# Kernel tuning notes

Measured on AMD Instinct MI355X. Metric: run time of the kernel, lower is better.

Reference implementation:

```python
import jax, jax.numpy as jnp
import numpy as np

NUM_HEADS = 24
HEAD_DIM = 64
SCALE = HEAD_DIM ** -0.5


def setup_inputs() -> dict:
    key = jax.random.key(0)
    ks = jax.random.split(key, 6)
    b, n_img, n_txt = 2, 4096, 128
    c_in, c_out, c_ctx = 1536, 1536, 4096
    x = jax.random.normal(ks[0], (b, n_img, c_in), dtype=jnp.float32)
    context = jax.random.normal(ks[1], (b, n_txt, c_ctx), dtype=jnp.float32)
    # realistic padding mask: first 96 of 128 tokens valid
    context_mask = jnp.broadcast_to(jnp.arange(n_txt) < 96, (b, n_txt))
    # Linear(in, out, bias=False) stored as [in, out] so y = x @ W
    Wq = jax.random.normal(ks[2], (c_in, c_out), dtype=jnp.float32) * (c_in ** -0.5)
    Wk = jax.random.normal(ks[3], (c_ctx, c_out), dtype=jnp.float32) * (c_ctx ** -0.5)
    Wv = jax.random.normal(ks[4], (c_ctx, c_out), dtype=jnp.float32) * (c_ctx ** -0.5)
    Wo = jax.random.normal(ks[5], (c_out, c_out), dtype=jnp.float32) * (c_out ** -0.5)
    return {"x": x, "context": context, "context_mask": context_mask,
            "Wq": Wq, "Wk": Wk, "Wv": Wv, "Wo": Wo}


def reference(x, context, context_mask, Wq, Wk, Wv, Wo):
    b, n, _ = x.shape
    h, d = NUM_HEADS, HEAD_DIM
    # project and split heads: b n (h d) -> b h n d
    q = (x @ Wq).reshape(b, n, h, d).transpose(0, 2, 1, 3)
    k = (context @ Wk).reshape(b, -1, h, d).transpose(0, 2, 1, 3)
    v = (context @ Wv).reshape(b, -1, h, d).transpose(0, 2, 1, 3)
    scores = jnp.einsum('bhid,bhjd->bhij', q, k) * SCALE
    max_neg = -jnp.finfo(scores.dtype).max
    scores = jnp.where(context_mask[:, None, None, :], scores, max_neg)
    attn = jax.nn.softmax(scores, axis=-1)
    out = jnp.einsum('bhij,bhjd->bhid', attn, v)
    out = out.transpose(0, 2, 1, 3).reshape(b, n, h * d)
    return out @ Wo
```

## Files before the change

kernel.cpp:

```cpp
#include <hip/hip_runtime.h>

typedef __attribute__((ext_vector_type(8))) short s8bf;
typedef __attribute__((ext_vector_type(8))) __bf16 v8bf;
typedef __attribute__((ext_vector_type(4))) float f32x4;

__device__ __forceinline__ short f2bf(float f) {
  union { float f; unsigned u; } v; v.f = f;
  unsigned r = v.u + 0x7FFFu + ((v.u >> 16) & 1u);
  return (short)(r >> 16);
}

__device__ __forceinline__ s8bf pack8(float4 a, float4 b) {
  s8bf o;
  o[0] = f2bf(a.x); o[1] = f2bf(a.y); o[2] = f2bf(a.z); o[3] = f2bf(a.w);
  o[4] = f2bf(b.x); o[5] = f2bf(b.y); o[6] = f2bf(b.z); o[7] = f2bf(b.w);
  return o;
}

__device__ __forceinline__ f32x4 mfma16(s8bf a, s8bf b, f32x4 c) {
  return __builtin_amdgcn_mfma_f32_16x16x32_bf16(
      __builtin_bit_cast(v8bf, a), __builtin_bit_cast(v8bf, b), c, 0, 0, 0);
}

__device__ __forceinline__ void gl_lds16(const void* g, void* l) {
  __builtin_amdgcn_global_load_lds(
      (const __attribute__((address_space(1))) unsigned*)g,
      (__attribute__((address_space(3))) unsigned*)l, 16, 0, 0);
}

__global__ __launch_bounds__(256) void cast_k(
    const float* __restrict__ x, const float* __restrict__ ctx,
    const void* __restrict__ msk,
    short* __restrict__ xbf, short* __restrict__ ctxbf, float* __restrict__ bias)
{
  __shared__ int fmt;
  const int blk = blockIdx.x;
  const int t = threadIdx.x;
  if (blk < 1664) {
    const float4* src;
    s8bf* dst;
    if (blk < 1536) { src = (const float4*)x + (size_t)blk * 2048;
                      dst = (s8bf*)xbf + (size_t)blk * 1024; }
    else            { src = (const float4*)ctx + (size_t)(blk - 1536) * 2048;
                      dst = (s8bf*)ctxbf + (size_t)(blk - 1536) * 1024; }
    float4 a0 = src[2 * t];        float4 b0 = src[2 * t + 1];
    float4 a1 = src[2 * t + 512];  float4 b1 = src[2 * t + 513];
    float4 a2 = src[2 * t + 1024]; float4 b2 = src[2 * t + 1025];
    float4 a3 = src[2 * t + 1536]; float4 b3 = src[2 * t + 1537];
    dst[t]       = pack8(a0, b0);
    dst[t + 256] = pack8(a1, b1);
    dst[t + 512] = pack8(a2, b2);
    dst[t + 768] = pack8(a3, b3);
  } else {
    const unsigned char* p8 = (const unsigned char*)msk;
    if (t == 0) {
      const float* pf = (const float*)msk;
      int allf = 1, anyone = 0;
      for (int i = 0; i < 64; ++i) {
        float f = pf[i];
        if (f != 0.0f && f != 1.0f) allf = 0;
        if (f == 1.0f) anyone = 1;
      }
      int any13 = 0;
      for (int i = 0; i < 256; ++i) if ((i & 3) && p8[i]) any13 = 1;
      fmt = (allf && anyone) ? 2 : (any13 ? 0 : 1);
    }
    __syncthreads();
    int j = t;
    if (j < 256) {
      int m;
      if (fmt == 2)      m = (((const float*)msk)[j] != 0.0f);
      else if (fmt == 0) m = (p8[j] != 0);
      else               m = (((const int*)msk)[j] != 0);
      bias[j] = m ? 0.0f : -1e30f;
    }
  }
}

__global__ __launch_bounds__(256) void transp_k(
    const float* __restrict__ Wq, const float* __restrict__ Wk,
    const float* __restrict__ Wv, const float* __restrict__ Wo,
    short* __restrict__ WqT, short* __restrict__ WkT,
    short* __restrict__ WvT, short* __restrict__ WoT)
{
  __shared__ float tile[64][65];
  int t = blockIdx.x;
  const float* W; short* Wt; int K, t0;
  if (t < 576)       { W = Wq; Wt = WqT; K = 1536; t0 = t; }
  else if (t < 2112) { W = Wk; Wt = WkT; K = 4096; t0 = t - 576; }
  else if (t < 3648) { W = Wv; Wt = WvT; K = 4096; t0 = t - 2112; }
  else               { W = Wo; Wt = WoT; K = 1536; t0 = t - 3648; }
  const int N = 1536;
  int ntx = K / 64;
  int k0 = (t0 % ntx) * 64, n0 = (t0 / ntx) * 64;
  int r = threadIdx.x >> 4;
  int c4 = threadIdx.x & 15;
  #pragma unroll
  for (int i = 0; i < 4; ++i) {
    float4 v = *(const float4*)(W + (size_t)(k0 + r + i * 16) * N + n0 + c4 * 4);
    tile[r + i * 16][c4 * 4 + 0] = v.x;
    tile[r + i * 16][c4 * 4 + 1] = v.y;
    tile[r + i * 16][c4 * 4 + 2] = v.z;
    tile[r + i * 16][c4 * 4 + 3] = v.w;
  }
  __syncthreads();
  int n = threadIdx.x >> 3, kc = threadIdx.x & 7;
  #pragma unroll
  for (int half = 0; half < 2; ++half) {
    int nn = n + half * 32;
    s8bf o;
    #pragma unroll
    for (int j = 0; j < 8; ++j) o[j] = f2bf(tile[kc * 8 + j][nn]);
    *(s8bf*)(Wt + (size_t)(n0 + nn) * K + k0 + kc * 8) = o;
  }
}

template<int MODE>
__global__ __launch_bounds__(512, 2) void gemm4ph_k(
    const short* __restrict__ A, const short* __restrict__ Bt, void* __restrict__ C,
    int M, int N, int K)
{
  extern __shared__ char ldsb[];
  const int tid = threadIdx.x, wid = tid >> 6, lane = tid & 63;
  const int nbx = N / 192;
  const int nwg = gridDim.x, bid = blockIdx.x;
  const int swz = (bid & 7) * (nwg >> 3) + (bid >> 3);
  const int m0 = (swz / nbx) * 256, n0 = (swz % nbx) * 192;
  const int wm = wid >> 2, wn = wid & 3;
  const int NT = K / 64;

  const int l = lane & 15, h = lane >> 4;
  const int rdslot = (((l & 1) * 4 + h) ^ (l >> 1)) * 16;
  int aoff[8], boff[3];
  #pragma unroll
  for (int mf = 0; mf < 8; ++mf)
    aoff[mf] = (wm * 64 + mf * 8 + (l >> 1)) * 128 + rdslot;
  #pragma unroll
  for (int nf = 0; nf < 3; ++nf)
    boff[nf] = 32768 + (wn * 24 + nf * 8 + (l >> 1)) * 128 + rdslot;

  const int ls = (tid & 7) ^ ((tid >> 3) & 7);
  const int srow2 = 2 * (tid >> 3) + (ls >> 2);
  const int scol = (ls & 3) * 8;
  const short* sA_lo = A  + (size_t)(m0 + srow2) * K + scol;
  const short* sA_hi = A  + (size_t)(m0 + 128 + srow2) * K + scol;
  const short* sB_lo = Bt + (size_t)(n0 + srow2) * K + scol;
  const short* sB_hi = Bt + (size_t)(n0 + 128 + srow2) * K + scol;
  const int d16 = tid * 16;

  f32x4 acc[8][3] = {};
  s8bf av[4], av2[4], bk[3];

  gl_lds16(sA_lo,      ldsb + 0     + d16);
  gl_lds16(sA_hi,      ldsb + 8192  + d16);
  gl_lds16(sB_lo,      ldsb + 32768 + d16);
  if (wid < 4) gl_lds16(sB_hi,      ldsb + 40960 + d16);
  gl_lds16(sA_lo + 32, ldsb + 16384 + d16);
  gl_lds16(sA_hi + 32, ldsb + 24576 + d16);
  gl_lds16(sB_lo + 32, ldsb + 45056 + d16);
  if (wid < 4) gl_lds16(sB_hi + 32, ldsb + 53248 + d16);
  gl_lds16(sA_lo + 64, ldsb + 57344 + 0     + d16);
  gl_lds16(sA_hi + 64, ldsb + 57344 + 8192  + d16);
  gl_lds16(sB_lo + 64, ldsb + 57344 + 32768 + d16);
  if (wid < 4) gl_lds16(sB_hi + 64, ldsb + 57344 + 40960 + d16);
  if (wid < 4) asm volatile("s_waitcnt vmcnt(8)" ::: "memory");
  else         asm volatile("s_waitcnt vmcnt(6)" ::: "memory");
  __builtin_amdgcn_s_barrier();

  for (int t = 0; t < NT; ++t) {
    const int bo = (t & 1) * 57344, bo2 = bo ^ 57344;
    const int kt1 = ((t + 1) < NT ? (t + 1) : (NT - 1)) * 64;
    const int kt2 = ((t + 2) < NT ? (t + 2) : (NT - 1)) * 64;
    #pragma unroll
    for (int i = 0; i < 4; ++i) av[i] = *(const s8bf*)(ldsb + bo + aoff[i]);
    #pragma unroll
    for (int nf = 0; nf < 3; ++nf) bk[nf] = *(const s8bf*)(ldsb + bo + boff[nf]);
    gl_lds16(sA_lo + kt1 + 32, ldsb + bo2 + 16384 + d16);
    gl_lds16(sA_hi + kt1 + 32, ldsb + bo2 + 24576 + d16);
    __builtin_amdgcn_s_barrier();
    asm volatile("s_waitcnt lgkmcnt(0)" ::: "memory");
    __builtin_amdgcn_s_setprio(1);
    #pragma unroll
    for (int i = 0; i < 4; ++i)
      #pragma unroll
      for (int nf = 0; nf < 3; ++nf)
        acc[i][nf] = mfma16(av[i], bk[nf], acc[i][nf]);
    __builtin_amdgcn_s_setprio(0);
    __builtin_amdgcn_s_barrier();
    #pragma unroll
    for (int i = 0; i < 4; ++i) av2[i] = *(const s8bf*)(ldsb + bo + aoff[4 + i]);
    gl_lds16(sB_lo + kt1 + 32, ldsb + bo2 + 45056 + d16);
    if (wid < 4) gl_lds16(sB_hi + kt1 + 32, ldsb + bo2 + 53248 + d16);
    __builtin_amdgcn_s_barrier();
    asm volatile("s_waitcnt lgkmcnt(0)" ::: "memory");
    __builtin_amdgcn_s_setprio(1);
    #pragma unroll
    for (int i = 0; i < 4; ++i)
      #pragma unroll
      for (int nf = 0; nf < 3; ++nf)
        acc[4 + i][nf] = mfma16(av2[i], bk[nf], acc[4 + i][nf]);
    __builtin_amdgcn_s_setprio(0);
    if (wid < 4) asm volatile("s_waitcnt vmcnt(8)" ::: "memory");
    else         asm volatile("s_waitcnt vmcnt(6)" ::: "memory");
    __builtin_amdgcn_s_barrier();
    #pragma unroll
    for (int i = 0; i < 4; ++i) av[i] = *(const s8bf*)(ldsb + bo + 16384 + aoff[i]);
    #pragma unroll
    for (int nf = 0; nf < 3; ++nf) bk[nf] = *(const s8bf*)(ldsb + bo + 12288 + boff[nf]);
    gl_lds16(sA_lo + kt2, ldsb + bo + 0    + d16);
    gl_lds16(sA_hi + kt2, ldsb + bo + 8192 + d16);
    __builtin_amdgcn_s_barrier();
    asm volatile("s_waitcnt lgkmcnt(0)" ::: "memory");
    __builtin_amdgcn_s_setprio(1);
    #pragma unroll
    for (int i = 0; i < 4; ++i)
      #pragma unroll
      for (int nf = 0; nf < 3; ++nf)
        acc[i][nf] = mfma16(av[i], bk[nf], acc[i][nf]);
    __builtin_amdgcn_s_setprio(0);
    __builtin_amdgcn_s_barrier();
    #pragma unroll
    for (int i = 0; i < 4; ++i) av2[i] = *(const s8bf*)(ldsb + bo + 16384 + aoff[4 + i]);
    gl_lds16(sB_lo + kt2, ldsb + bo + 32768 + d16);
    if (wid < 4) gl_lds16(sB_hi + kt2, ldsb + bo + 40960 + d16);
    __builtin_amdgcn_s_barrier();
    asm volatile("s_waitcnt lgkmcnt(0)" ::: "memory");
    __builtin_amdgcn_s_setprio(1);
    #pragma unroll
    for (int i = 0; i < 4; ++i)
      #pragma unroll
      for (int nf = 0; nf < 3; ++nf)
        acc[4 + i][nf] = mfma16(av2[i], bk[nf], acc[4 + i][nf]);
    __builtin_amdgcn_s_setprio(0);
    if (wid < 4) asm volatile("s_waitcnt vmcnt(8)" ::: "memory");
    else         asm volatile("s_waitcnt vmcnt(6)" ::: "memory");
    __builtin_amdgcn_s_barrier();
  }
  asm volatile("s_waitcnt vmcnt(0)" ::: "memory");

  const int r0 = m0 + wm * 128 + ((lane >> 4) << 2);
  const int c0 = n0 + wn * 48 + (lane & 15);
  #pragma unroll
  for (int mf = 0; mf < 8; ++mf)
    #pragma unroll
    for (int nf = 0; nf < 3; ++nf)
      #pragma unroll
      for (int v = 0; v < 4; ++v) {
        int row = r0 + mf * 16 + v, col = c0 + nf * 16;
        float val = acc[mf][nf][v];
        if (MODE == 0) ((short*)C)[(size_t)row * N + col] = f2bf(val);
        else           ((float*)C)[(size_t)row * N + col] = val;
      }
}

template<int MODE>
__global__ __launch_bounds__(256, 2) void gemm_bt_k(
    const short* __restrict__ A, const short* __restrict__ Bt, void* __restrict__ C,
    int M, int N, int K, int kchunk)
{
  __shared__ short aT[128 * 32];
  __shared__ short bT[128 * 32];
  const int m0 = blockIdx.x * 128, n0 = blockIdx.y * 128;
  const int wid = threadIdx.x >> 6, lane = threadIdx.x & 63;
  const int wr = wid >> 1, wc = wid & 1;
  const int k_lo = blockIdx.z * kchunk, k_hi = k_lo + kchunk;
  f32x4 acc[4][4] = {};
  const int srow = wid * 32 + (lane >> 2);
  const int skoff = (lane & 3) * 8;
  const short* aG = A + (size_t)(m0 + srow) * K + skoff;
  const short* bG = Bt + (size_t)(n0 + srow) * K + skoff;
  char* aL = (char*)aT + wid * 2048;
  char* bL = (char*)bT + wid * 2048;
  const short* ap = aT + (wr * 64 + (lane & 15)) * 32 + (lane >> 4) * 8;
  const short* bp = bT + (wc * 64 + (lane & 15)) * 32 + (lane >> 4) * 8;
  for (int k0 = k_lo; k0 < k_hi; k0 += 32) {
    gl_lds16(aG + k0, aL);
    gl_lds16(aG + (size_t)16 * K + k0, aL + 1024);
    gl_lds16(bG + k0, bL);
    gl_lds16(bG + (size_t)16 * K + k0, bL + 1024);
    __syncthreads();
    s8bf af[4], bf[4];
    #pragma unroll
    for (int i = 0; i < 4; ++i) {
      af[i] = *(const s8bf*)(ap + i * 512);
      bf[i] = *(const s8bf*)(bp + i * 512);
    }
    #pragma unroll
    for (int mi = 0; mi < 4; ++mi)
      #pragma unroll
      for (int ni = 0; ni < 4; ++ni)
        acc[mi][ni] = mfma16(af[mi], bf[ni], acc[mi][ni]);
    __syncthreads();
  }
  const int r0 = m0 + wr * 64 + ((lane >> 4) << 2);
  const int c0 = n0 + wc * 64 + (lane & 15);
  float* Cf = (float*)C + (size_t)blockIdx.z * 786432;
  #pragma unroll
  for (int mi = 0; mi < 4; ++mi)
    #pragma unroll
    for (int ni = 0; ni < 4; ++ni)
      #pragma unroll
      for (int v = 0; v < 4; ++v) {
        int row = r0 + mi * 16 + v, col = c0 + ni * 16;
        Cf[(size_t)row * N + col] = acc[mi][ni][v];
      }
}

__global__ void kv_reduce_k(const float* __restrict__ part, short* __restrict__ kbf,
                            short* __restrict__ vtbf) {
  int t = blockIdx.x * 256 + threadIdx.x;
  int row = t / 768, c4 = (t % 768) * 4;
  float4 s = {0.f, 0.f, 0.f, 0.f};
  const float* p = part + (size_t)row * 3072 + c4;
  #pragma unroll
  for (int z = 0; z < 8; ++z) {
    float4 v = *(const float4*)(p + (size_t)z * 786432);
    s.x += v.x; s.y += v.y; s.z += v.z; s.w += v.w;
  }
  if (c4 < 1536) {
    short4 o = { f2bf(s.x), f2bf(s.y), f2bf(s.z), f2bf(s.w) };
    *(short4*)(kbf + (size_t)row * 1536 + c4) = o;
  } else {
    int b = row >> 7, j = row & 127, c = c4 - 1536;
    vtbf[((size_t)(b * 1536 + c + 0)) * 128 + j] = f2bf(s.x);
    vtbf[((size_t)(b * 1536 + c + 1)) * 128 + j] = f2bf(s.y);
    vtbf[((size_t)(b * 1536 + c + 2)) * 128 + j] = f2bf(s.z);
    vtbf[((size_t)(b * 1536 + c + 3)) * 128 + j] = f2bf(s.w);
  }
}

__global__ __launch_bounds__(256, 3) void attn_k(
    const short* __restrict__ q, const short* __restrict__ kk,
    const short* __restrict__ vt, const float* __restrict__ bias,
    short* __restrict__ ao)
{
  __shared__ char sm_[49152];
  const int it = blockIdx.x, h = blockIdx.y, b = blockIdx.z;
  const int wid = threadIdx.x >> 6, lane = threadIdx.x & 63;
  const int i0 = it * 128;
  char* kT = sm_;
  char* vT = sm_ + 16384;
  char* pB = (wid < 2) ? (sm_ + wid * 8192) : (sm_ + 16384 + wid * 8192);

  #pragma unroll
  for (int c = 0; c < 4; ++c) {
    int seg = c * 256 + wid * 64 + lane;
    int j = seg >> 3, ds = seg & 7;
    int dsrc = ds ^ (j & 7);
    gl_lds16(kk + ((size_t)(b * 128 + j) * 1536 + h * 64 + dsrc * 8),
             kT + c * 4096 + wid * 1024);
  }
  #pragma unroll
  for (int c = 0; c < 4; ++c) {
    int seg = c * 256 + wid * 64 + lane;
    int d = seg >> 4, js = seg & 15;
    int jsrc = js ^ (d & 7);
    gl_lds16(vt + ((size_t)(b * 1536 + h * 64 + d) * 128 + jsrc * 8),
             vT + c * 4096 + wid * 1024);
  }

  float bcol[8];
  #pragma unroll
  for (int nj = 0; nj < 8; ++nj) bcol[nj] = bias[b * 128 + nj * 16 + (lane & 15)];

  s8bf qf[2][2];
  #pragma unroll
  for (int mi = 0; mi < 2; ++mi)
    #pragma unroll
    for (int ks = 0; ks < 2; ++ks) {
      size_t row = (size_t)(b * 4096 + i0 + wid * 32 + mi * 16 + (lane & 15));
      qf[mi][ks] = *(const s8bf*)(q + row * 1536 + h * 64 + ks * 32 + (lane >> 4) * 8);
    }
  __syncthreads();

  f32x4 s[2][8] = {};
  #pragma unroll
  for (int ks = 0; ks < 2; ++ks) {
    int kd = ks * 32 + (lane >> 4) * 8;
    #pragma unroll
    for (int nj = 0; nj < 8; ++nj) {
      int j = nj * 16 + (lane & 15);
      s8bf kb = *(const s8bf*)(kT + j * 128 + ((2 * kd) ^ ((j & 7) << 4)));
      s[0][nj] = mfma16(qf[0][ks], kb, s[0][nj]);
      s[1][nj] = mfma16(qf[1][ks], kb, s[1][nj]);
    }
  }
  __syncthreads();

  float sm[2][4];
  #pragma unroll
  for (int mi = 0; mi < 2; ++mi)
    #pragma unroll
    for (int v = 0; v < 4; ++v) {
      float mx = -1e30f;
      #pragma unroll
      for (int nj = 0; nj < 8; ++nj) {
        float sv = s[mi][nj][v] * 0.125f + bcol[nj];
        s[mi][nj][v] = sv;
        mx = fmaxf(mx, sv);
      }
      mx = fmaxf(mx, __shfl_xor(mx, 1));
      mx = fmaxf(mx, __shfl_xor(mx, 2));
      mx = fmaxf(mx, __shfl_xor(mx, 4));
      mx = fmaxf(mx, __shfl_xor(mx, 8));
      float ss = 0.f;
      #pragma unroll
      for (int nj = 0; nj < 8; ++nj) {
        float p = __expf(s[mi][nj][v] - mx);
        s[mi][nj][v] = p;
        ss += p;
      }
      ss += __shfl_xor(ss, 1);
      ss += __shfl_xor(ss, 2);
      ss += __shfl_xor(ss, 4);
      ss += __shfl_xor(ss, 8);
      sm[mi][v] = ss;
    }

  #pragma unroll
  for (int mi = 0; mi < 2; ++mi)
    #pragma unroll
    for (int v = 0; v < 4; ++v) {
      int r = mi * 16 + ((lane >> 4) << 2) + v;
      char* base = pB + r * 256;
      #pragma unroll
      for (int nj = 0; nj < 8; ++nj) {
        int j = nj * 16 + (lane & 15);
        *(short*)(base + ((2 * j) ^ ((r & 7) << 4))) = f2bf(s[mi][nj][v]);
      }
    }
  __syncthreads();

  f32x4 o_[2][4] = {};
  #pragma unroll
  for (int ks = 0; ks < 4; ++ks) {
    int j = ks * 32 + (lane >> 4) * 8;
    s8bf pa[2];
    #pragma unroll
    for (int mi = 0; mi < 2; ++mi) {
      int r = mi * 16 + (lane & 15);
      pa[mi] = *(const s8bf*)(pB + r * 256 + ((2 * j) ^ ((r & 7) << 4)));
    }
    #pragma unroll
    for (int dj = 0; dj < 4; ++dj) {
      int d = dj * 16 + (lane & 15);
      s8bf vb = *(const s8bf*)(vT + d * 256 + ((2 * j) ^ ((d & 7) << 4)));
      o_[0][dj] = mfma16(pa[0], vb, o_[0][dj]);
      o_[1][dj] = mfma16(pa[1], vb, o_[1][dj]);
    }
  }

  #pragma unroll
  for (int mi = 0; mi < 2; ++mi)
    #pragma unroll
    for (int v = 0; v < 4; ++v) {
      int r = mi * 16 + ((lane >> 4) << 2) + v;
      float is = 1.0f / sm[mi][v];
      size_t row = (size_t)(b * 4096 + i0 + wid * 32 + r);
      #pragma unroll
      for (int dj = 0; dj < 4; ++dj) {
        int d = dj * 16 + (lane & 15);
        ao[row * 1536 + h * 64 + d] = f2bf(o_[mi][dj][v] * is);
      }
    }
}

extern "C" void kernel_launch(void* const* d_in, const int* in_sizes, int n_in,
                              void* d_out, int out_size, void* d_ws, size_t ws_size,
                              hipStream_t stream) {
  const float* x   = (const float*)d_in[0];
  const float* ctx = (const float*)d_in[1];
  const void*  msk = d_in[2];
  const float* Wq  = (const float*)d_in[3];
  const float* Wk  = (const float*)d_in[4];
  const float* Wv  = (const float*)d_in[5];
  const float* Wo  = (const float*)d_in[6];
  float* out = (float*)d_out;

  const int B = 2, NI = 4096, NT = 128, C = 1536, CC = 4096, H = 24;
  const int Mq = B * NI;
  const int Mk = B * NT;

  size_t off = 0;
  auto carve = [&](size_t bytes) -> void* {
    void* p = (char*)d_ws + off;
    off += (bytes + 255) & ~(size_t)255;
    return p;
  };
  short* xbf   = (short*)carve((size_t)Mq * C * 2);
  short* ctxbf = (short*)carve((size_t)Mk * CC * 2);
  short* WqT   = (short*)carve((size_t)C * C * 2);
  short* WkT   = (short*)carve((size_t)CC * C * 2);
  short* WvT   = (short*)carve((size_t)CC * C * 2);
  short* WoT   = (short*)carve((size_t)C * C * 2);
  short* qbf   = (short*)carve((size_t)Mq * C * 2);
  short* kbf   = (short*)carve((size_t)Mk * C * 2);
  short* vtbf  = (short*)carve((size_t)Mk * C * 2);
  float* bias  = (float*)carve(256 * 4);
  short* aout  = xbf;
  float* part  = out;

  hipFuncSetAttribute((const void*)gemm4ph_k<0>, hipFuncAttributeMaxDynamicSharedMemorySize, 114688);
  hipFuncSetAttribute((const void*)gemm4ph_k<1>, hipFuncAttributeMaxDynamicSharedMemorySize, 114688);

  cast_k<<<1665, 256, 0, stream>>>(x, ctx, msk, xbf, ctxbf, bias);
  transp_k<<<4224, 256, 0, stream>>>(Wq, Wk, Wv, Wo, WqT, WkT, WvT, WoT);

  gemm4ph_k<0><<<(Mq / 256) * (C / 192), 512, 114688, stream>>>(xbf, WqT, qbf, Mq, C, C);
  gemm_bt_k<5><<<dim3(Mk / 128, 3072 / 128, 8), 256, 0, stream>>>(ctxbf, WkT, part, Mk, 3072, CC, 512);
  kv_reduce_k<<<768, 256, 0, stream>>>(part, kbf, vtbf);

  attn_k<<<dim3(NI / 128, H, B), 256, 0, stream>>>(qbf, kbf, vtbf, bias, aout);

  gemm4ph_k<1><<<(Mq / 256) * (C / 192), 512, 114688, stream>>>(aout, WoT, out, Mq, C, C);
}
```

Baseline: 168.6 us.

## Shrink Q/O projection GEMM tile to 128x192 with four-wave workgroups

The Q and output projection GEMMs change from 256x192 tiles with 8 waves to 128x192 tiles with 4 waves. Each wave now covers all 128 rows and a 48-column slice, and the LDS staging layout, prefetch lambdas, wait counts and LDS size (81920 bytes) are rebuilt to match. The aim is twice as many workgroups for M=8192, giving better CU fill and a smaller tail across the 256 CUs, plus less LDS per block so more blocks can be resident. The cost is less data reuse per tile, so more global and L2 traffic for the B operand.

```diff
diff --git a/kernel.cpp b/kernel.cpp
--- a/kernel.cpp
+++ b/kernel.cpp
@@ -116,7 +116,7 @@
 }
 
 template<int MODE>
-__global__ __launch_bounds__(512, 2) void gemm4ph_k(
+__global__ __launch_bounds__(256, 2) void gemm4ph_k(
     const short* __restrict__ A, const short* __restrict__ Bt, void* __restrict__ C,
     int M, int N, int K)
 {
@@ -125,8 +125,7 @@
   const int nbx = N / 192;
   const int nwg = gridDim.x, bid = blockIdx.x;
   const int swz = (bid & 7) * (nwg >> 3) + (bid >> 3);
-  const int m0 = (swz / nbx) * 256, n0 = (swz % nbx) * 192;
-  const int wm = wid >> 2, wn = wid & 3;
+  const int m0 = (swz / nbx) * 128, n0 = (swz % nbx) * 192;
   const int NT = K / 64;
 
   const int l = lane & 15, h = lane >> 4;
@@ -134,49 +133,59 @@
   int aoff[8], boff[3];
   #pragma unroll
   for (int mf = 0; mf < 8; ++mf)
-    aoff[mf] = (wm * 64 + mf * 8 + (l >> 1)) * 128 + rdslot;
+    aoff[mf] = (mf * 8 + (l >> 1)) * 128 + rdslot;
   #pragma unroll
   for (int nf = 0; nf < 3; ++nf)
-    boff[nf] = 32768 + (wn * 24 + nf * 8 + (l >> 1)) * 128 + rdslot;
+    boff[nf] = 16384 + (wid * 24 + nf * 8 + (l >> 1)) * 128 + rdslot;
 
   const int ls = (tid & 7) ^ ((tid >> 3) & 7);
   const int srow2 = 2 * (tid >> 3) + (ls >> 2);
   const int scol = (ls & 3) * 8;
-  const short* sA_lo = A  + (size_t)(m0 + srow2) * K + scol;
-  const short* sA_hi = A  + (size_t)(m0 + 128 + srow2) * K + scol;
-  const short* sB_lo = Bt + (size_t)(n0 + srow2) * K + scol;
-  const short* sB_hi = Bt + (size_t)(n0 + 128 + srow2) * K + scol;
+  const short* sA0 = A  + (size_t)(m0 + srow2) * K + scol;
+  const short* sA1 = A  + (size_t)(m0 + 64 + srow2) * K + scol;
+  const short* sB0 = Bt + (size_t)(n0 + srow2) * K + scol;
+  const short* sB1 = Bt + (size_t)(n0 + 64 + srow2) * K + scol;
+  const short* sB2 = Bt + (size_t)(n0 + 128 + srow2) * K + scol;
   const int d16 = tid * 16;
+
+  auto stA0 = [&](int ko, int bo_) {
+    gl_lds16(sA0 + ko, ldsb + bo_ + 0    + d16);
+    gl_lds16(sA1 + ko, ldsb + bo_ + 4096 + d16);
+  };
+  auto stA1 = [&](int ko, int bo_) {
+    gl_lds16(sA0 + ko + 32, ldsb + bo_ + 8192  + d16);
+    gl_lds16(sA1 + ko + 32, ldsb + bo_ + 12288 + d16);
+  };
+  auto stB0 = [&](int ko, int bo_) {
+    gl_lds16(sB0 + ko, ldsb + bo_ + 16384 + d16);
+    gl_lds16(sB1 + ko, ldsb + bo_ + 20480 + d16);
+    gl_lds16(sB2 + ko, ldsb + bo_ + 24576 + d16);
+  };
+  auto stB1 = [&](int ko, int bo_) {
+    gl_lds16(sB0 + ko + 32, ldsb + bo_ + 28672 + d16);
+    gl_lds16(sB1 + ko + 32, ldsb + bo_ + 32768 + d16);
+    gl_lds16(sB2 + ko + 32, ldsb + bo_ + 36864 + d16);
+  };
 
   f32x4 acc[8][3] = {};
   s8bf av[4], av2[4], bk[3];
 
-  gl_lds16(sA_lo,      ldsb + 0     + d16);
-  gl_lds16(sA_hi,      ldsb + 8192  + d16);
-  gl_lds16(sB_lo,      ldsb + 32768 + d16);
-  if (wid < 4) gl_lds16(sB_hi,      ldsb + 40960 + d16);
-  gl_lds16(sA_lo + 32, ldsb + 16384 + d16);
-  gl_lds16(sA_hi + 32, ldsb + 24576 + d16);
-  gl_lds16(sB_lo + 32, ldsb + 45056 + d16);
-  if (wid < 4) gl_lds16(sB_hi + 32, ldsb + 53248 + d16);
-  gl_lds16(sA_lo + 64, ldsb + 57344 + 0     + d16);
-  gl_lds16(sA_hi + 64, ldsb + 57344 + 8192  + d16);
-  gl_lds16(sB_lo + 64, ldsb + 57344 + 32768 + d16);
-  if (wid < 4) gl_lds16(sB_hi + 64, ldsb + 57344 + 40960 + d16);
-  if (wid < 4) asm volatile("s_waitcnt vmcnt(8)" ::: "memory");
-  else         asm volatile("s_waitcnt vmcnt(6)" ::: "memory");
+  stA0(0, 0); stB0(0, 0);
+  stA1(0, 0); stB1(0, 0);
+  const int k1 = ((1 < NT) ? 1 : 0) * 64;
+  stA0(k1, 40960); stB0(k1, 40960);
+  asm volatile("s_waitcnt vmcnt(10)" ::: "memory");
   __builtin_amdgcn_s_barrier();
 
   for (int t = 0; t < NT; ++t) {
-    const int bo = (t & 1) * 57344, bo2 = bo ^ 57344;
+    const int bo = (t & 1) * 40960, bo2 = bo ^ 40960;
     const int kt1 = ((t + 1) < NT ? (t + 1) : (NT - 1)) * 64;
     const int kt2 = ((t + 2) < NT ? (t + 2) : (NT - 1)) * 64;
     #pragma unroll
     for (int i = 0; i < 4; ++i) av[i] = *(const s8bf*)(ldsb + bo + aoff[i]);
     #pragma unroll
     for (int nf = 0; nf < 3; ++nf) bk[nf] = *(const s8bf*)(ldsb + bo + boff[nf]);
-    gl_lds16(sA_lo + kt1 + 32, ldsb + bo2 + 16384 + d16);
-    gl_lds16(sA_hi + kt1 + 32, ldsb + bo2 + 24576 + d16);
+    stA1(kt1, bo2);
     __builtin_amdgcn_s_barrier();
     asm volatile("s_waitcnt lgkmcnt(0)" ::: "memory");
     __builtin_amdgcn_s_setprio(1);
@@ -189,8 +198,7 @@
     __builtin_amdgcn_s_barrier();
     #pragma unroll
     for (int i = 0; i < 4; ++i) av2[i] = *(const s8bf*)(ldsb + bo + aoff[4 + i]);
-    gl_lds16(sB_lo + kt1 + 32, ldsb + bo2 + 45056 + d16);
-    if (wid < 4) gl_lds16(sB_hi + kt1 + 32, ldsb + bo2 + 53248 + d16);
+    stB1(kt1, bo2);
     __builtin_amdgcn_s_barrier();
     asm volatile("s_waitcnt lgkmcnt(0)" ::: "memory");
     __builtin_amdgcn_s_setprio(1);
@@ -200,15 +208,13 @@
       for (int nf = 0; nf < 3; ++nf)
         acc[4 + i][nf] = mfma16(av2[i], bk[nf], acc[4 + i][nf]);
     __builtin_amdgcn_s_setprio(0);
-    if (wid < 4) asm volatile("s_waitcnt vmcnt(8)" ::: "memory");
-    else         asm volatile("s_waitcnt vmcnt(6)" ::: "memory");
-    __builtin_amdgcn_s_barrier();
-    #pragma unroll
-    for (int i = 0; i < 4; ++i) av[i] = *(const s8bf*)(ldsb + bo + 16384 + aoff[i]);
+    asm volatile("s_waitcnt vmcnt(10)" ::: "memory");
+    __builtin_amdgcn_s_barrier();
+    #pragma unroll
+    for (int i = 0; i < 4; ++i) av[i] = *(const s8bf*)(ldsb + bo + 8192 + aoff[i]);
     #pragma unroll
     for (int nf = 0; nf < 3; ++nf) bk[nf] = *(const s8bf*)(ldsb + bo + 12288 + boff[nf]);
-    gl_lds16(sA_lo + kt2, ldsb + bo + 0    + d16);
-    gl_lds16(sA_hi + kt2, ldsb + bo + 8192 + d16);
+    stA0(kt2, bo);
     __builtin_amdgcn_s_barrier();
     asm volatile("s_waitcnt lgkmcnt(0)" ::: "memory");
     __builtin_amdgcn_s_setprio(1);
@@ -220,9 +226,8 @@
     __builtin_amdgcn_s_setprio(0);
     __builtin_amdgcn_s_barrier();
     #pragma unroll
-    for (int i = 0; i < 4; ++i) av2[i] = *(const s8bf*)(ldsb + bo + 16384 + aoff[4 + i]);
-    gl_lds16(sB_lo + kt2, ldsb + bo + 32768 + d16);
-    if (wid < 4) gl_lds16(sB_hi + kt2, ldsb + bo + 40960 + d16);
+    for (int i = 0; i < 4; ++i) av2[i] = *(const s8bf*)(ldsb + bo + 8192 + aoff[4 + i]);
+    stB0(kt2, bo);
     __builtin_amdgcn_s_barrier();
     asm volatile("s_waitcnt lgkmcnt(0)" ::: "memory");
     __builtin_amdgcn_s_setprio(1);
@@ -232,14 +237,13 @@
       for (int nf = 0; nf < 3; ++nf)
         acc[4 + i][nf] = mfma16(av2[i], bk[nf], acc[4 + i][nf]);
     __builtin_amdgcn_s_setprio(0);
-    if (wid < 4) asm volatile("s_waitcnt vmcnt(8)" ::: "memory");
-    else         asm volatile("s_waitcnt vmcnt(6)" ::: "memory");
+    asm volatile("s_waitcnt vmcnt(10)" ::: "memory");
     __builtin_amdgcn_s_barrier();
   }
   asm volatile("s_waitcnt vmcnt(0)" ::: "memory");
 
-  const int r0 = m0 + wm * 128 + ((lane >> 4) << 2);
-  const int c0 = n0 + wn * 48 + (lane & 15);
+  const int r0 = m0 + ((lane >> 4) << 2);
+  const int c0 = n0 + wid * 48 + (lane & 15);
   #pragma unroll
   for (int mf = 0; mf < 8; ++mf)
     #pragma unroll
@@ -500,17 +504,17 @@
   short* aout  = xbf;
   float* part  = out;
 
-  hipFuncSetAttribute((const void*)gemm4ph_k<0>, hipFuncAttributeMaxDynamicSharedMemorySize, 114688);
-  hipFuncSetAttribute((const void*)gemm4ph_k<1>, hipFuncAttributeMaxDynamicSharedMemorySize, 114688);
+  hipFuncSetAttribute((const void*)gemm4ph_k<0>, hipFuncAttributeMaxDynamicSharedMemorySize, 81920);
+  hipFuncSetAttribute((const void*)gemm4ph_k<1>, hipFuncAttributeMaxDynamicSharedMemorySize, 81920);
 
   cast_k<<<1665, 256, 0, stream>>>(x, ctx, msk, xbf, ctxbf, bias);
   transp_k<<<4224, 256, 0, stream>>>(Wq, Wk, Wv, Wo, WqT, WkT, WvT, WoT);
 
-  gemm4ph_k<0><<<(Mq / 256) * (C / 192), 512, 114688, stream>>>(xbf, WqT, qbf, Mq, C, C);
+  gemm4ph_k<0><<<(Mq / 128) * (C / 192), 256, 81920, stream>>>(xbf, WqT, qbf, Mq, C, C);
   gemm_bt_k<5><<<dim3(Mk / 128, 3072 / 128, 8), 256, 0, stream>>>(ctxbf, WkT, part, Mk, 3072, CC, 512);
   kv_reduce_k<<<768, 256, 0, stream>>>(part, kbf, vtbf);
 
   attn_k<<<dim3(NI / 128, H, B), 256, 0, stream>>>(qbf, kbf, vtbf, bias, aout);
 
-  gemm4ph_k<1><<<(Mq / 256) * (C / 192), 512, 114688, stream>>>(aout, WoT, out, Mq, C, C);
-}
+  gemm4ph_k<1><<<(Mq / 128) * (C / 192), 256, 81920, stream>>>(aout, WoT, out, Mq, C, C);
+}
```

After: 172.0 us. No clear change (+2.0%).
